# Optimization experiments

Hardware: AMD Instinct MI355X
Metric: run time of the kernel (lower is better)

## Reference

```python
import jax, jax.numpy as jnp
import numpy as np

B, S, D, H = 2, 2048, 1024, 16
HD = D // H


def setup_inputs() -> dict:
    key = jax.random.key(0)
    ks = jax.random.split(key, 9)
    s = 1.0 / np.sqrt(D)
    return {
        "qx": jax.random.normal(ks[0], (B, S, D), jnp.float32),
        "kx": jax.random.normal(ks[1], (B, S, D), jnp.float32),
        "vx": jax.random.normal(ks[2], (B, S, D), jnp.float32),
        "mask": jnp.tril(jnp.ones((S, S), jnp.int32))[None, None],  # [1,1,S,S] causal
        "Wq": jax.random.uniform(ks[3], (D, D), jnp.float32, -s, s),
        "bq": jax.random.uniform(ks[4], (D,), jnp.float32, -s, s),
        "Wk": jax.random.uniform(ks[5], (D, D), jnp.float32, -s, s),
        "bk": jax.random.uniform(ks[6], (D,), jnp.float32, -s, s),
        "Wv": jax.random.uniform(ks[7], (D, D), jnp.float32, -s, s),
        "bv": jax.random.uniform(ks[8], (D,), jnp.float32, -s, s),
    }


def reference(qx, kx, vx, mask, Wq, bq, Wk, bk, Wv, bv):
    bat, seq_len, d_model = qx.shape
    # torch Linear: y = x @ W.T + b
    q = qx @ Wq.T + bq
    k = kx @ Wk.T + bk
    v = vx @ Wv.T + bv
    # [b, h, s, hd]
    q = q.reshape(bat, seq_len, H, HD).transpose(0, 2, 1, 3)
    k = k.reshape(bat, seq_len, H, HD).transpose(0, 2, 1, 3)
    v = v.reshape(bat, seq_len, H, HD).transpose(0, 2, 1, 3)
    # NOTE: original scales by sqrt(d_model), not sqrt(head_dim)
    attn_weight = jnp.einsum('bhqd,bhkd->bhqk', q, k) / jnp.sqrt(
        jnp.asarray(d_model, q.dtype))
    attn_weight = jnp.where(mask == 0, -jnp.inf, attn_weight)
    attn_score = jax.nn.softmax(attn_weight, axis=-1)
    attn_output = jnp.einsum('bhqk,bhkd->bhqd', attn_score, v)
    return attn_output.transpose(0, 2, 1, 3).reshape(bat, seq_len, d_model)
```

## Files before the change

### kernel.cpp

```cpp
#include <hip/hip_runtime.h>


typedef __attribute__((ext_vector_type(8))) short short8;
typedef __attribute__((ext_vector_type(4))) short shortx4;
typedef __attribute__((ext_vector_type(4))) float floatx4;
typedef __attribute__((ext_vector_type(2))) unsigned int uintx2;

#define NEGBIG (-1.0e30f)
#define QSCALE 0.04508422002778011f
#define SLOTF 4160

__device__ __forceinline__ float bf2f(ushort u) {
    union { unsigned int i; float f; } x; x.i = ((unsigned int)u) << 16; return x.f;
}
__device__ __forceinline__ ushort f2bf(float f) {
    union { unsigned int i; float f; } x; x.f = f;
    return (ushort)((x.i + 0x7FFFu + ((x.i >> 16) & 1u)) >> 16);
}
__device__ __forceinline__ void gl_lds16(const void* g, void* l) {
    __builtin_amdgcn_global_load_lds(
        (const __attribute__((address_space(1))) unsigned int*)g,
        (__attribute__((address_space(3))) unsigned int*)l, 16, 0, 0);
}

__global__ void convert_fp32(
    const float* __restrict__ qx, const float* __restrict__ kx, const float* __restrict__ vx,
    const float* __restrict__ wq, const float* __restrict__ wk, const float* __restrict__ wv,
    const float* __restrict__ bq, const float* __restrict__ bk, const float* __restrict__ bv,
    ushort* __restrict__ dst, int* __restrict__ flag)
{
    const unsigned int* w = (const unsigned int*)qx;
    int hits = 0;
#pragma unroll
    for (int i = 0; i < 4; ++i) {
        unsigned int v = w[threadIdx.x * 4 + i];
        int e = (int)((v >> 7) & 0xFF);
        hits += (e >= 100 && e <= 135) ? 1 : 0;
    }
    __shared__ int red[4];
    for (int off = 32; off; off >>= 1) hits += __shfl_down(hits, off);
    if ((threadIdx.x & 63) == 0) red[threadIdx.x >> 6] = hits;
    __syncthreads();
    const int dt = (red[0] + red[1] + red[2] + red[3] > 512) ? 1 : 0;
    if (blockIdx.x == 0 && threadIdx.x == 0) *flag = dt;
    if (dt) return;

    const int v = blockIdx.x * 256 + threadIdx.x;
    const float* src; int off = v;
    if      (v < 1048576) { src = qx; }
    else if (v < 2097152) { src = kx; off = v - 1048576; }
    else if (v < 3145728) { src = vx; off = v - 2097152; }
    else if (v < 3407872) { src = wq; off = v - 3145728; }
    else if (v < 3670016) { src = wk; off = v - 3407872; }
    else if (v < 3932160) { src = wv; off = v - 3670016; }
    else if (v < 3932416) { src = bq; off = v - 3932160; }
    else if (v < 3932672) { src = bk; off = v - 3932416; }
    else                  { src = bv; off = v - 3932672; }
    float4 f = ((const float4*)src)[off];
    shortx4 o;
    o[0] = (short)f2bf(f.x); o[1] = (short)f2bf(f.y);
    o[2] = (short)f2bf(f.z); o[3] = (short)f2bf(f.w);
    *(shortx4*)&dst[(size_t)v * 4] = o;
}

__global__ __launch_bounds__(256, 4) void qkv_gemm(
    const void* __restrict__ Xq_, const void* __restrict__ Wq_, const void* __restrict__ bq_,
    const void* __restrict__ Xk_, const void* __restrict__ Wk_, const void* __restrict__ bk_,
    const void* __restrict__ Xv_, const void* __restrict__ Wv_, const void* __restrict__ bv_,
    const ushort* __restrict__ conv,
    ushort* __restrict__ Yq, ushort* __restrict__ Yk, ushort* __restrict__ Yv,
    const int* __restrict__ flag)
{
    const int idx = blockIdx.x;
    const int xcd = idx & 7;
    const int j   = (idx >> 3) & 7;
    const int pg  = idx >> 6;
    const int p   = pg * 8 + xcd;
    const int z   = p >> 5;
    const int m0  = (p & 31) * 128;
    const int n0  = j * 128;

    const int dt = *flag;
    const ushort* X = dt ? (const ushort*)(z == 0 ? Xq_ : z == 1 ? Xk_ : Xv_)
                         : conv + (size_t)z * 4194304;
    const ushort* W = dt ? (const ushort*)(z == 0 ? Wq_ : z == 1 ? Wk_ : Wv_)
                         : conv + 12582912 + (size_t)z * 1048576;
    const ushort* bias = dt ? (const ushort*)(z == 0 ? bq_ : z == 1 ? bk_ : bv_)
                            : conv + 15728640 + z * 1024;
    ushort* Y = (z == 0) ? Yq : (z == 1) ? Yk : Yv;
    const float oscale = (z == 0) ? QSCALE : 1.0f;

    __shared__ __align__(16) ushort As[128 * 64];
    __shared__ __align__(16) ushort Bs[128 * 64];

    const int tid  = threadIdx.x;
    const int wave = tid >> 6;
    const int lane = tid & 63;
    const int col  = lane & 15;
    const int quad = lane >> 4;
    const int wm   = (wave >> 1) * 64;
    const int wn   = (wave & 1) * 64;

    floatx4 acc[4][4] = {};

    for (int k0 = 0; k0 < 1024; k0 += 64) {
        __syncthreads();
#pragma unroll
        for (int c = 0; c < 4; ++c) {
            const int o   = c * 4096 + tid * 16;
            const int row = o >> 7;
            const int bg  = ((o >> 4) & 7) ^ (row & 7);
            gl_lds16(X + (size_t)(m0 + row) * 1024 + k0 + bg * 8, &As[o >> 1]);
            gl_lds16(W + (size_t)(n0 + row) * 1024 + k0 + bg * 8, &Bs[o >> 1]);
        }
        __syncthreads();

#pragma unroll
        for (int h = 0; h < 2; ++h) {
            short8 af[4], bf_[4];
#pragma unroll
            for (int i = 0; i < 4; ++i) {
                const int ra = wm + i * 16 + col;
                const int rb = wn + i * 16 + col;
                af[i]  = *(const short8*)&As[ra * 64 + (((h * 4 + quad) ^ (ra & 7)) * 8)];
                bf_[i] = *(const short8*)&Bs[rb * 64 + (((h * 4 + quad) ^ (rb & 7)) * 8)];
            }
#pragma unroll
            for (int i = 0; i < 4; ++i)
#pragma unroll
                for (int jj = 0; jj < 4; ++jj)
                    acc[i][jj] = __builtin_amdgcn_mfma_f32_16x16x32_bf16(af[i], bf_[jj], acc[i][jj], 0, 0, 0);
        }
    }

    if (z == 2) {
#pragma unroll
        for (int jj = 0; jj < 4; ++jj) {
            const int n = n0 + wn + jj * 16 + col;
            const float bb = bf2f(bias[n]);
#pragma unroll
            for (int i = 0; i < 4; ++i) {
                const int m = m0 + wm + i * 16 + quad * 4;
                shortx4 pk;
#pragma unroll
                for (int r = 0; r < 4; ++r) pk[r] = (short)f2bf(acc[i][jj][r] + bb);
                *(shortx4*)&Y[((size_t)(m >> 11) * 1024 + n) * 2048 + (m & 2047)] = pk;
            }
        }
    } else {
#pragma unroll
        for (int jj = 0; jj < 4; ++jj) {
            const int n = n0 + wn + jj * 16 + col;
            const float bb = bf2f(bias[n]);
#pragma unroll
            for (int i = 0; i < 4; ++i)
#pragma unroll
                for (int r = 0; r < 4; ++r) {
                    const int m = m0 + wm + i * 16 + quad * 4 + r;
                    Y[(size_t)m * 1024 + n] = f2bf((acc[i][jj][r] + bb) * oscale);
                }
        }
    }
}

__global__ __launch_bounds__(256, 4) void attn(
    const ushort* __restrict__ Q, const ushort* __restrict__ K,
    const ushort* __restrict__ Vt, void* __restrict__ O,
    float* __restrict__ PW, const int* __restrict__ flag)
{
    const int i   = blockIdx.x;
    const int xcd = i & 7;
    const int m   = i >> 3;
    const int run = m & 3;
    const int jm  = m >> 2;
    int qt, chunk, n;
    if (jm < 30)      { qt = 31 - jm / 3;        chunk = jm % 3;        n = 3; }
    else if (jm < 52) { qt = 21 - (jm - 30) / 2; chunk = (jm - 30) % 2; n = 2; }
    else              { qt = 10 - (jm - 52);     chunk = 0;             n = 1; }
    const int T  = qt + 1;
    const int t0 = chunk * T / n;
    const int t1 = (chunk + 1) * T / n;

    const int g   = xcd + 8 * run;
    const int b   = g >> 4;
    const int h   = g & 15;
    const int q0  = qt * 64;
    const int dt  = *flag;

    __shared__ __align__(16) ushort SH[20480];

    const int tid  = threadIdx.x;
    const int wv   = tid >> 6;
    const int lane = tid & 63;
    const int col  = lane & 15;
    const int quad = lane >> 4;
    const int wq   = wv >> 1;
    const int wk   = wv & 1;

    const size_t qkbase = ((size_t)b * 2048) * 1024 + h * 64;
    const size_t vtbase = ((size_t)(b * 16 + h) * 64) * 2048;

    short8 ones;
#pragma unroll
    for (int ii = 0; ii < 8; ++ii) ones[ii] = (short)0x3F80;

    const int o0   = tid * 16;
    const int o1   = 4096 + tid * 16;
    const int row0 = o0 >> 7, row1 = o1 >> 7;
    const int bg0  = ((o0 >> 4) & 7) ^ (row0 & 7);
    const int bg1  = ((o1 >> 4) & 7) ^ (row1 & 7);

    short8 qf[2][2];
#pragma unroll
    for (int mt = 0; mt < 2; ++mt) {
        const int rq = wq * 32 + mt * 16 + col;
#pragma unroll
        for (int hf = 0; hf < 2; ++hf)
            qf[mt][hf] = *(const short8*)&Q[qkbase + (size_t)(q0 + rq) * 1024 + hf * 32 + quad * 8];
    }

    const ushort* kg0 = K  + qkbase + (size_t)(t0 * 64 + row0) * 1024 + bg0 * 8;
    const ushort* kg1 = K  + qkbase + (size_t)(t0 * 64 + row1) * 1024 + bg1 * 8;
    const ushort* vg0 = Vt + vtbase + (size_t)row0 * 2048 + t0 * 64 + bg0 * 8;
    const ushort* vg1 = Vt + vtbase + (size_t)row1 * 2048 + t0 * 64 + bg1 * 8;

#define PREF(BUF) do {                                                        \
        gl_lds16(kg0, &SH[(BUF) * 4096 + (o0 >> 1)]);                         \
        gl_lds16(kg1, &SH[(BUF) * 4096 + (o1 >> 1)]);                         \
        gl_lds16(vg0, &SH[8192 + (BUF) * 4096 + (o0 >> 1)]);                  \
        gl_lds16(vg1, &SH[8192 + (BUF) * 4096 + (o1 >> 1)]);                  \
        kg0 += 65536; kg1 += 65536; vg0 += 64; vg1 += 64;                     \
    } while (0)

    floatx4 oacc[2][4] = {};
    floatx4 sacc[2] = {};

    ushort* Pw = &SH[16384 + wv * 1024];

#define COMPUTE(TT, BUF) do {                                                 \
        const ushort* Kc = &SH[(BUF) * 4096];                                 \
        const ushort* Vc = &SH[8192 + (BUF) * 4096];                          \
        short8 kf[2][2];                                                      \
        _Pragma("unroll")                                                     \
        for (int nt = 0; nt < 2; ++nt) {                                      \
            const int rk = wk * 32 + nt * 16 + col;                           \
            _Pragma("unroll")                                                 \
            for (int hf = 0; hf < 2; ++hf)                                    \
                kf[nt][hf] = *(const short8*)&Kc[rk * 64 + (((hf * 4 + quad) ^ (col & 7)) * 8)]; \
        }                                                                     \
        floatx4 s4[2][2];                                                     \
        __builtin_amdgcn_s_setprio(1);                                        \
        _Pragma("unroll")                                                     \
        for (int mt = 0; mt < 2; ++mt)                                        \
            _Pragma("unroll")                                                 \
            for (int nt = 0; nt < 2; ++nt) {                                  \
                floatx4 a = {};                                               \
                a = __builtin_amdgcn_mfma_f32_16x16x32_bf16(kf[nt][0], qf[mt][0], a, 0, 0, 0); \
                a = __builtin_amdgcn_mfma_f32_16x16x32_bf16(kf[nt][1], qf[mt][1], a, 0, 0, 0); \
                s4[mt][nt] = a;                                               \
            }                                                                 \
        __builtin_amdgcn_s_setprio(0);                                        \
        if ((TT) == qt) {                                                     \
            _Pragma("unroll")                                                 \
            for (int mt = 0; mt < 2; ++mt) {                                  \
                const int qix = wq * 32 + mt * 16 + col;                      \
                _Pragma("unroll")                                             \
                for (int nt = 0; nt < 2; ++nt)                                \
                    _Pragma("unroll")                                         \
                    for (int r = 0; r < 4; ++r) {                             \
                        const int kix = wk * 32 + nt * 16 + quad * 4 + r;     \
                        s4[mt][nt][r] = (kix <= qix) ? s4[mt][nt][r] : NEGBIG; \
                    }                                                         \
            }                                                                 \
        }                                                                     \
        short8 pf[2];                                                         \
        _Pragma("unroll")                                                     \
        for (int mt = 0; mt < 2; ++mt) {                                      \
            const int row = mt * 16 + col;                                    \
            const int sw  = (row + (row >> 2)) & 3;                           \
            _Pragma("unroll")                                                 \
            for (int nt = 0; nt < 2; ++nt) {                                  \
                float e0 = __builtin_exp2f(s4[mt][nt][0]);                    \
                float e1 = __builtin_exp2f(s4[mt][nt][1]);                    \
                float e2 = __builtin_exp2f(s4[mt][nt][2]);                    \
                float e3 = __builtin_exp2f(s4[mt][nt][3]);                    \
                unsigned int lo, hi;                                          \
                asm("v_cvt_pk_bf16_f32 %0, %1, %2" : "=v"(lo) : "v"(e0), "v"(e1)); \
                asm("v_cvt_pk_bf16_f32 %0, %1, %2" : "=v"(hi) : "v"(e2), "v"(e3)); \
                const int bpos = (nt * 2 + (quad >> 1)) ^ sw;                 \
                *(uintx2*)&Pw[row * 32 + bpos * 8 + (quad & 1) * 4] = (uintx2){lo, hi}; \
            }                                                                 \
            pf[mt] = *(const short8*)&Pw[row * 32 + ((quad ^ sw) * 8)];       \
        }                                                                     \
        __builtin_amdgcn_s_setprio(1);                                        \
        sacc[0] = __builtin_amdgcn_mfma_f32_16x16x32_bf16(pf[0], ones, sacc[0], 0, 0, 0); \
        sacc[1] = __builtin_amdgcn_mfma_f32_16x16x32_bf16(pf[1], ones, sacc[1], 0, 0, 0); \
        _Pragma("unroll")                                                     \
        for (int ct = 0; ct < 4; ++ct) {                                      \
            const int rv = ct * 16 + col;                                     \
            short8 vf = *(const short8*)&Vc[rv * 64 + (((wk * 4 + quad) ^ (col & 7)) * 8)]; \
            oacc[0][ct] = __builtin_amdgcn_mfma_f32_16x16x32_bf16(pf[0], vf, oacc[0][ct], 0, 0, 0); \
            oacc[1][ct] = __builtin_amdgcn_mfma_f32_16x16x32_bf16(pf[1], vf, oacc[1][ct], 0, 0, 0); \
        }                                                                     \
        __builtin_amdgcn_s_setprio(0);                                        \
    } while (0)

    PREF(0);
    __syncthreads();

    int tcur = t0;
    int nrem = t1 - t0;
    while (nrem >= 2) {
        PREF(1);
        COMPUTE(tcur, 0);
        __syncthreads();
        if (nrem > 2) PREF(0);
        COMPUTE(tcur + 1, 1);
        if (nrem > 2) __syncthreads();
        tcur += 2; nrem -= 2;
    }
    if (nrem == 1) COMPUTE(tcur, 0);

#undef PREF
#undef COMPUTE

    __syncthreads();
    float* scr = (float*)SH;
    if (wk == 1) {
        float* s = scr + wq * 2080;
#pragma unroll
        for (int mt = 0; mt < 2; ++mt) {
#pragma unroll
            for (int ct = 0; ct < 4; ++ct)
#pragma unroll
                for (int r = 0; r < 4; ++r)
                    s[(mt * 16 + quad * 4 + r) * 64 + ct * 16 + col] = oacc[mt][ct][r];
            if (col == 0)
#pragma unroll
                for (int r = 0; r < 4; ++r)
                    s[2048 + mt * 16 + quad * 4 + r] = sacc[mt][r];
        }
    }
    __syncthreads();
    if (wk == 0) {
        float* s = scr + wq * 2080;
#pragma unroll
        for (int mt = 0; mt < 2; ++mt) {
#pragma unroll
            for (int ct = 0; ct < 4; ++ct)
#pragma unroll
                for (int r = 0; r < 4; ++r)
                    oacc[mt][ct][r] += s[(mt * 16 + quad * 4 + r) * 64 + ct * 16 + col];
#pragma unroll
            for (int r = 0; r < 4; ++r)
                sacc[mt][r] += s[2048 + mt * 16 + quad * 4 + r];
        }

        if (n == 1) {
#pragma unroll
            for (int mt = 0; mt < 2; ++mt)
#pragma unroll
                for (int r = 0; r < 4; ++r) {
                    const float inv = 1.0f / sacc[mt][r];
                    const int q = q0 + wq * 32 + mt * 16 + quad * 4 + r;
#pragma unroll
                    for (int ct = 0; ct < 4; ++ct) {
                        const float v = oacc[mt][ct][r] * inv;
                        const size_t oidx = ((size_t)b * 2048 + q) * 1024 + h * 64 + ct * 16 + col;
                        if (dt) ((ushort*)O)[oidx] = f2bf(v);
                        else    ((float*)O)[oidx]  = v;
                    }
                }
        } else {
            const int sl = (qt <= 21) ? (qt - 11) * 2 + chunk : 22 + (qt - 22) * 3 + chunk;
            float* slot = PW + ((size_t)g * 52 + sl) * SLOTF;
#pragma unroll
            for (int mt = 0; mt < 2; ++mt)
#pragma unroll
                for (int r = 0; r < 4; ++r) {
                    const int pr = wq * 32 + mt * 16 + quad * 4 + r;
#pragma unroll
                    for (int ct = 0; ct < 4; ++ct)
                        slot[pr * 64 + ct * 16 + col] = oacc[mt][ct][r];
                    if (col == 0) slot[4096 + pr] = sacc[mt][r];
                }
        }
    }
}

__global__ __launch_bounds__(256) void attn_combine(
    const float* __restrict__ PW, void* __restrict__ O, const int* __restrict__ flag)
{
    const int c  = blockIdx.x;
    const int g  = c & 31;
    const int qi = c >> 5;
    const int qt = 11 + qi;
    const int n  = (qt <= 21) ? 2 : 3;
    const int b  = g >> 4, h = g & 15;
    const int sl0 = (qt <= 21) ? (qt - 11) * 2 : 22 + (qt - 22) * 3;
    const float* base = PW + ((size_t)g * 52 + sl0) * SLOTF;

    const int t   = threadIdx.x;
    const int row = t >> 2;
    const int c0  = (t & 3) * 16;

    float acc[16] = {};
    float l = 0.0f;
    for (int s = 0; s < n; ++s) {
        const float* sp = base + (size_t)s * SLOTF;
        l += sp[4096 + row];
#pragma unroll
        for (int k = 0; k < 16; k += 4) {
            float4 v = *(const float4*)&sp[row * 64 + c0 + k];
            acc[k] += v.x; acc[k + 1] += v.y; acc[k + 2] += v.z; acc[k + 3] += v.w;
        }
    }
    const float inv = 1.0f / l;
    const int dt = *flag;
    const size_t o0 = ((size_t)b * 2048 + qt * 64 + row) * 1024 + h * 64 + c0;
    if (dt) {
#pragma unroll
        for (int k = 0; k < 16; ++k) ((ushort*)O)[o0 + k] = f2bf(acc[k] * inv);
    } else {
#pragma unroll
        for (int k = 0; k < 16; ++k) ((float*)O)[o0 + k] = acc[k] * inv;
    }
}

extern "C" void kernel_launch(void* const* d_in, const int* in_sizes, int n_in,
                              void* d_out, int out_size, void* d_ws, size_t ws_size,
                              hipStream_t stream) {
    const void* qx = d_in[0];
    const void* kx = d_in[1];
    const void* vx = d_in[2];
    const void* Wq = d_in[4]; const void* bq = d_in[5];
    const void* Wk = d_in[6]; const void* bk = d_in[7];
    const void* Wv = d_in[8]; const void* bv = d_in[9];

    int*    flag = (int*)d_ws;
    ushort* conv = (ushort*)((char*)d_ws + 256);
    ushort* Qw   = (ushort*)((char*)d_ws + 256 + 31463424);
    ushort* Kw   = Qw + (size_t)4096 * 1024;
    ushort* Vtw  = Kw + (size_t)4096 * 1024;
    float*  PW   = (float*)conv;

    convert_fp32<<<15363, 256, 0, stream>>>(
        (const float*)qx, (const float*)kx, (const float*)vx,
        (const float*)Wq, (const float*)Wk, (const float*)Wv,
        (const float*)bq, (const float*)bk, (const float*)bv, conv, flag);

    qkv_gemm<<<768, 256, 0, stream>>>(qx, Wq, bq, kx, Wk, bk, vx, Wv, bv,
                                      conv, Qw, Kw, Vtw, flag);

    attn<<<2016, 256, 0, stream>>>(Qw, Kw, Vtw, d_out, PW, flag);

    attn_combine<<<672, 256, 0, stream>>>(PW, d_out, flag);
}
```

Before: 206.2 us.

## Enlarge attention query tile to 128 rows with 512-thread blocks

The attention kernel now processes 128 query rows per block using 8 waves and 512 threads, so each K/V tile staged in LDS is reused by twice as many query rows. The causal split-K schedule, slot indexing and the combine kernel are redone for the 16 query blocks. The padded LDS stride used in the reduction scratch changes from 64 to 68 to avoid bank conflicts. In exchange there are fewer blocks, so load balance across CUs is coarser, and the diagonal masking now covers two 64-key tiles per wave group.

```diff
diff --git a/kernel.cpp b/kernel.cpp
--- a/kernel.cpp
+++ b/kernel.cpp
@@ -8,7 +8,7 @@
 
 #define NEGBIG (-1.0e30f)
 #define QSCALE 0.04508422002778011f
-#define SLOTF 4160
+#define SLOTF 8320
 
 __device__ __forceinline__ float bf2f(ushort u) {
     union { unsigned int i; float f; } x; x.i = ((unsigned int)u) << 16; return x.f;
@@ -163,7 +163,7 @@
     }
 }
 
-__global__ __launch_bounds__(256, 4) void attn(
+__global__ __launch_bounds__(512, 6) void attn(
     const ushort* __restrict__ Q, const ushort* __restrict__ K,
     const ushort* __restrict__ Vt, void* __restrict__ O,
     float* __restrict__ PW, const int* __restrict__ flag)
@@ -173,21 +173,20 @@
     const int m   = i >> 3;
     const int run = m & 3;
     const int jm  = m >> 2;
-    int qt, chunk, n;
-    if (jm < 30)      { qt = 31 - jm / 3;        chunk = jm % 3;        n = 3; }
-    else if (jm < 52) { qt = 21 - (jm - 30) / 2; chunk = (jm - 30) % 2; n = 2; }
-    else              { qt = 10 - (jm - 52);     chunk = 0;             n = 1; }
-    const int T  = qt + 1;
+    int qb, chunk, n;
+    if (jm < 15)      { qb = 15 - jm / 3;        chunk = jm % 3;        n = 3; }
+    else if (jm < 27) { qb = 10 - (jm - 15) / 2; chunk = (jm - 15) % 2; n = 2; }
+    else              { qb = 4 - (jm - 27);      chunk = 0;             n = 1; }
+    const int T  = 2 * qb + 2;
     const int t0 = chunk * T / n;
     const int t1 = (chunk + 1) * T / n;
 
     const int g   = xcd + 8 * run;
     const int b   = g >> 4;
     const int h   = g & 15;
-    const int q0  = qt * 64;
     const int dt  = *flag;
 
-    __shared__ __align__(16) ushort SH[20480];
+    __shared__ __align__(16) ushort SH[24576];
 
     const int tid  = threadIdx.x;
     const int wv   = tid >> 6;
@@ -197,6 +196,9 @@
     const int wq   = wv >> 1;
     const int wk   = wv & 1;
 
+    const int qtw = 2 * qb + (wq >> 1);
+    const int qgw = qb * 128 + wq * 32;
+
     const size_t qkbase = ((size_t)b * 2048) * 1024 + h * 64;
     const size_t vtbase = ((size_t)(b * 16 + h) * 64) * 2048;
 
@@ -204,32 +206,25 @@
 #pragma unroll
     for (int ii = 0; ii < 8; ++ii) ones[ii] = (short)0x3F80;
 
-    const int o0   = tid * 16;
-    const int o1   = 4096 + tid * 16;
-    const int row0 = o0 >> 7, row1 = o1 >> 7;
-    const int bg0  = ((o0 >> 4) & 7) ^ (row0 & 7);
-    const int bg1  = ((o1 >> 4) & 7) ^ (row1 & 7);
+    const int srow = tid >> 3;
+    const int sbg  = (tid & 7) ^ (srow & 7);
+    const int so   = tid * 8;
 
     short8 qf[2][2];
 #pragma unroll
     for (int mt = 0; mt < 2; ++mt) {
-        const int rq = wq * 32 + mt * 16 + col;
 #pragma unroll
         for (int hf = 0; hf < 2; ++hf)
-            qf[mt][hf] = *(const short8*)&Q[qkbase + (size_t)(q0 + rq) * 1024 + hf * 32 + quad * 8];
-    }
-
-    const ushort* kg0 = K  + qkbase + (size_t)(t0 * 64 + row0) * 1024 + bg0 * 8;
-    const ushort* kg1 = K  + qkbase + (size_t)(t0 * 64 + row1) * 1024 + bg1 * 8;
-    const ushort* vg0 = Vt + vtbase + (size_t)row0 * 2048 + t0 * 64 + bg0 * 8;
-    const ushort* vg1 = Vt + vtbase + (size_t)row1 * 2048 + t0 * 64 + bg1 * 8;
+            qf[mt][hf] = *(const short8*)&Q[qkbase + (size_t)(qgw + mt * 16 + col) * 1024 + hf * 32 + quad * 8];
+    }
+
+    const ushort* kg = K  + qkbase + (size_t)(t0 * 64 + srow) * 1024 + sbg * 8;
+    const ushort* vg = Vt + vtbase + (size_t)srow * 2048 + t0 * 64 + sbg * 8;
 
 #define PREF(BUF) do {                                                        \
-        gl_lds16(kg0, &SH[(BUF) * 4096 + (o0 >> 1)]);                         \
-        gl_lds16(kg1, &SH[(BUF) * 4096 + (o1 >> 1)]);                         \
-        gl_lds16(vg0, &SH[8192 + (BUF) * 4096 + (o0 >> 1)]);                  \
-        gl_lds16(vg1, &SH[8192 + (BUF) * 4096 + (o1 >> 1)]);                  \
-        kg0 += 65536; kg1 += 65536; vg0 += 64; vg1 += 64;                     \
+        gl_lds16(kg, &SH[(BUF) * 4096 + so]);                                 \
+        gl_lds16(vg, &SH[8192 + (BUF) * 4096 + so]);                          \
+        kg += 65536; vg += 64;                                                \
     } while (0)
 
     floatx4 oacc[2][4] = {};
@@ -260,16 +255,17 @@
                 s4[mt][nt] = a;                                               \
             }                                                                 \
         __builtin_amdgcn_s_setprio(0);                                        \
-        if ((TT) == qt) {                                                     \
+        if ((TT) >= qtw) {                                                    \
+            const int lim = qgw - (TT) * 64;                                  \
             _Pragma("unroll")                                                 \
             for (int mt = 0; mt < 2; ++mt) {                                  \
-                const int qix = wq * 32 + mt * 16 + col;                      \
+                const int qloc = mt * 16 + col;                               \
                 _Pragma("unroll")                                             \
                 for (int nt = 0; nt < 2; ++nt)                                \
                     _Pragma("unroll")                                         \
                     for (int r = 0; r < 4; ++r) {                             \
                         const int kix = wk * 32 + nt * 16 + quad * 4 + r;     \
-                        s4[mt][nt][r] = (kix <= qix) ? s4[mt][nt][r] : NEGBIG; \
+                        s4[mt][nt][r] = (kix <= qloc + lim) ? s4[mt][nt][r] : NEGBIG; \
                     }                                                         \
             }                                                                 \
         }                                                                     \
@@ -327,33 +323,33 @@
     __syncthreads();
     float* scr = (float*)SH;
     if (wk == 1) {
-        float* s = scr + wq * 2080;
+        float* s = scr + wq * 2208;
 #pragma unroll
         for (int mt = 0; mt < 2; ++mt) {
 #pragma unroll
             for (int ct = 0; ct < 4; ++ct)
 #pragma unroll
                 for (int r = 0; r < 4; ++r)
-                    s[(mt * 16 + quad * 4 + r) * 64 + ct * 16 + col] = oacc[mt][ct][r];
+                    s[(mt * 16 + quad * 4 + r) * 68 + ct * 16 + col] = oacc[mt][ct][r];
             if (col == 0)
 #pragma unroll
                 for (int r = 0; r < 4; ++r)
-                    s[2048 + mt * 16 + quad * 4 + r] = sacc[mt][r];
+                    s[2176 + mt * 16 + quad * 4 + r] = sacc[mt][r];
         }
     }
     __syncthreads();
     if (wk == 0) {
-        float* s = scr + wq * 2080;
+        float* s = scr + wq * 2208;
 #pragma unroll
         for (int mt = 0; mt < 2; ++mt) {
 #pragma unroll
             for (int ct = 0; ct < 4; ++ct)
 #pragma unroll
                 for (int r = 0; r < 4; ++r)
-                    oacc[mt][ct][r] += s[(mt * 16 + quad * 4 + r) * 64 + ct * 16 + col];
+                    oacc[mt][ct][r] += s[(mt * 16 + quad * 4 + r) * 68 + ct * 16 + col];
 #pragma unroll
             for (int r = 0; r < 4; ++r)
-                sacc[mt][r] += s[2048 + mt * 16 + quad * 4 + r];
+                sacc[mt][r] += s[2176 + mt * 16 + quad * 4 + r];
         }
 
         if (n == 1) {
@@ -362,7 +358,7 @@
 #pragma unroll
                 for (int r = 0; r < 4; ++r) {
                     const float inv = 1.0f / sacc[mt][r];
-                    const int q = q0 + wq * 32 + mt * 16 + quad * 4 + r;
+                    const int q = qgw + mt * 16 + quad * 4 + r;
 #pragma unroll
                     for (int ct = 0; ct < 4; ++ct) {
                         const float v = oacc[mt][ct][r] * inv;
@@ -372,8 +368,8 @@
                     }
                 }
         } else {
-            const int sl = (qt <= 21) ? (qt - 11) * 2 + chunk : 22 + (qt - 22) * 3 + chunk;
-            float* slot = PW + ((size_t)g * 52 + sl) * SLOTF;
+            const int sl = (qb <= 10) ? (qb - 5) * 2 + chunk : 12 + (qb - 11) * 3 + chunk;
+            float* slot = PW + ((size_t)g * 27 + sl) * SLOTF;
 #pragma unroll
             for (int mt = 0; mt < 2; ++mt)
 #pragma unroll
@@ -382,7 +378,7 @@
 #pragma unroll
                     for (int ct = 0; ct < 4; ++ct)
                         slot[pr * 64 + ct * 16 + col] = oacc[mt][ct][r];
-                    if (col == 0) slot[4096 + pr] = sacc[mt][r];
+                    if (col == 0) slot[8192 + pr] = sacc[mt][r];
                 }
         }
     }
@@ -394,30 +390,31 @@
     const int c  = blockIdx.x;
     const int g  = c & 31;
     const int qi = c >> 5;
-    const int qt = 11 + qi;
-    const int n  = (qt <= 21) ? 2 : 3;
+    const int qb = 5 + (qi >> 1);
+    const int hf = qi & 1;
+    const int n  = (qb <= 10) ? 2 : 3;
     const int b  = g >> 4, h = g & 15;
-    const int sl0 = (qt <= 21) ? (qt - 11) * 2 : 22 + (qt - 22) * 3;
-    const float* base = PW + ((size_t)g * 52 + sl0) * SLOTF;
+    const int sl0 = (qb <= 10) ? (qb - 5) * 2 : 12 + (qb - 11) * 3;
+    const float* base = PW + ((size_t)g * 27 + sl0) * SLOTF;
 
     const int t   = threadIdx.x;
-    const int row = t >> 2;
+    const int pr  = hf * 64 + (t >> 2);
     const int c0  = (t & 3) * 16;
 
     float acc[16] = {};
     float l = 0.0f;
     for (int s = 0; s < n; ++s) {
         const float* sp = base + (size_t)s * SLOTF;
-        l += sp[4096 + row];
+        l += sp[8192 + pr];
 #pragma unroll
         for (int k = 0; k < 16; k += 4) {
-            float4 v = *(const float4*)&sp[row * 64 + c0 + k];
+            float4 v = *(const float4*)&sp[pr * 64 + c0 + k];
             acc[k] += v.x; acc[k + 1] += v.y; acc[k + 2] += v.z; acc[k + 3] += v.w;
         }
     }
     const float inv = 1.0f / l;
     const int dt = *flag;
-    const size_t o0 = ((size_t)b * 2048 + qt * 64 + row) * 1024 + h * 64 + c0;
+    const size_t o0 = ((size_t)b * 2048 + qb * 128 + pr) * 1024 + h * 64 + c0;
     if (dt) {
 #pragma unroll
         for (int k = 0; k < 16; ++k) ((ushort*)O)[o0 + k] = f2bf(acc[k] * inv);
@@ -452,7 +449,7 @@
     qkv_gemm<<<768, 256, 0, stream>>>(qx, Wq, bq, kx, Wk, bk, vx, Wv, bv,
                                       conv, Qw, Kw, Vtw, flag);
 
-    attn<<<2016, 256, 0, stream>>>(Qw, Kw, Vtw, d_out, PW, flag);
-
-    attn_combine<<<672, 256, 0, stream>>>(PW, d_out, flag);
-}
+    attn<<<1024, 512, 0, stream>>>(Qw, Kw, Vtw, d_out, PW, flag);
+
+    attn_combine<<<704, 256, 0, stream>>>(PW, d_out, flag);
+}
```

Measured after the change: 299.9 us. 1.45x slower.
